# Performance work log

Hardware: AMD Instinct MI355X
Metric: run time of the kernel (lower is better)

## Reference

```python
import jax, jax.numpy as jnp
import numpy as np

N_HEADS = 16


def setup_inputs() -> dict:
    key = jax.random.key(0)
    k1, k2, k3, k4, k5 = jax.random.split(key, 5)
    B, S, D = 2, 2048, 1024
    return {
        "query": jax.random.normal(k1, (B, S, D), dtype=jnp.float32),
        "key": jax.random.normal(k2, (B, S, D), dtype=jnp.float32),
        "value": jax.random.normal(k3, (B, S, D), dtype=jnp.float32),
        "fc_w": jax.random.normal(k4, (D, D), dtype=jnp.float32) * (1.0 / np.sqrt(D)),
        "fc_b": jax.random.normal(k5, (D,), dtype=jnp.float32) * 0.01,
    }


def reference(query, key, value, fc_w, fc_b):
    b, s, d = query.shape
    head_dim = d // N_HEADS
    q = query.reshape(b, s, N_HEADS, head_dim)
    k = key.reshape(b, s, N_HEADS, head_dim)
    v = value.reshape(b, s, N_HEADS, head_dim)
    # energy: [b, n, q, k]
    energy = jnp.einsum('bqnd,bknd->bnqk', q, k)
    scale = 1.0 / jnp.sqrt(jnp.asarray(head_dim, dtype=energy.dtype))
    attn = jax.nn.softmax(energy * scale, axis=3)
    out = jnp.einsum('bnqk,bknd->bqnd', attn, v).reshape(b, s, d)
    # fc: y = x @ W^T + b (torch Linear convention)
    return out @ fc_w.T + fc_b
```

## Files before the change

### kernel.cpp

```cpp
#include <hip/hip_runtime.h>
#include <hip/hip_bf16.h>

#define BATCH 2
#define SEQ 2048
#define DMODEL 1024
#define NHEADS 16
#define HDIM 64
#define KVBLK 64
#define NCHUNK (SEQ / KVBLK)
#define NITER (NCHUNK / 2)

#define QSCALE 0.180336880f
#define DEFER_THR 8.0f

typedef __bf16 bf16x8 __attribute__((ext_vector_type(8)));
typedef __bf16 bf16x4 __attribute__((ext_vector_type(4)));
typedef float f32x4 __attribute__((ext_vector_type(4)));
typedef float f32x16 __attribute__((ext_vector_type(16)));
typedef unsigned int uint2v __attribute__((ext_vector_type(2)));

union B8u { unsigned int u[4]; bf16x8 v; };

__device__ __forceinline__ unsigned int cvt_pk_bf16(float lo, float hi) {
  unsigned int d;
  asm("v_cvt_pk_bf16_f32 %0, %1, %2" : "=v"(d) : "v"(lo), "v"(hi));
  return d;
}

__device__ __forceinline__ void permlane32_swap(unsigned &a, unsigned &b) {
  auto r = __builtin_amdgcn_permlane32_swap(a, b, false, false);
  unsigned tmp[2];
  __builtin_memcpy(tmp, &r, 8);
  a = tmp[0]; b = tmp[1];
}

__global__ __launch_bounds__(256)
void conv_k(const float* __restrict__ K, __bf16* __restrict__ Kbf) {
  const int t = blockIdx.x * 256 + threadIdx.x;
  const int d8 = t & 7, key = (t >> 3) & (SEQ - 1), g = t >> 14;
  const float* src = K + ((size_t)(g >> 4) * SEQ + key) * DMODEL +
                     (g & 15) * HDIM + d8 * 8;
  f32x4 a = *reinterpret_cast<const f32x4*>(src);
  f32x4 c = *reinterpret_cast<const f32x4*>(src + 4);
  bf16x8 o;
#pragma unroll
  for (int j = 0; j < 4; ++j) { o[j] = (__bf16)a[j]; o[4 + j] = (__bf16)c[j]; }
  *reinterpret_cast<bf16x8*>(Kbf + (size_t)t * 8) = o;
}

__global__ __launch_bounds__(256)
void conv_vt(const float* __restrict__ V, __bf16* __restrict__ Vt) {
  const int blk = blockIdx.x;
  const int g = blk >> 5, c0 = (blk & 31) * 64;
  const int b = g >> 4, h = g & 15;
  __shared__ __bf16 T[64][72];

  {
    const int key = threadIdx.x >> 2, dq = threadIdx.x & 3;
    const float* src = V + ((size_t)(b * SEQ) + c0 + key) * DMODEL +
                       h * HDIM + dq * 16;
#pragma unroll
    for (int i = 0; i < 4; ++i) {
      f32x4 v = *reinterpret_cast<const f32x4*>(src + 4 * i);
      bf16x4 o;
#pragma unroll
      for (int j = 0; j < 4; ++j) o[j] = (__bf16)v[j];
      *reinterpret_cast<bf16x4*>(&T[key][dq * 16 + 4 * i]) = o;
    }
  }
  __syncthreads();
  {
    const int d = threadIdx.x >> 2, kq = threadIdx.x & 3;
    bf16x8 r0, r1;
#pragma unroll
    for (int i = 0; i < 8; ++i) {
      r0[i] = T[kq * 16 + i][d];
      r1[i] = T[kq * 16 + 8 + i][d];
    }
    __bf16* dst = Vt + ((size_t)g * HDIM + d) * SEQ + c0 + kq * 16;
    *reinterpret_cast<bf16x8*>(dst) = r0;
    *reinterpret_cast<bf16x8*>(dst + 8) = r1;
  }
}

__global__ __launch_bounds__(256)
void conv_w(const float* __restrict__ W, __bf16* __restrict__ Wbf) {
  const int t = blockIdx.x * 256 + threadIdx.x;
  f32x4 a = *reinterpret_cast<const f32x4*>(W + (size_t)t * 8);
  f32x4 c = *reinterpret_cast<const f32x4*>(W + (size_t)t * 8 + 4);
  bf16x8 o;
#pragma unroll
  for (int j = 0; j < 4; ++j) { o[j] = (__bf16)a[j]; o[4 + j] = (__bf16)c[j]; }
  *reinterpret_cast<bf16x8*>(Wbf + (size_t)t * 8) = o;
}

__global__ __launch_bounds__(512, 4)
void attn_kernel(const float* __restrict__ Q, const __bf16* __restrict__ Kbf,
                 const __bf16* __restrict__ Vt, __bf16* __restrict__ O) {
  const int p = blockIdx.x;
  const int xcd = p & 7, slot = p >> 3;
  const int g = xcd + 8 * (slot >> 4);
  const int b = g >> 4, h = g & 15;
  const int q0 = (slot & 15) * 128;

  const int tid = threadIdx.x;
  const int wave = tid >> 6, lane = tid & 63;
  const int qg = wave & 3, ks = wave >> 2;
  const int l31 = lane & 31, hi = lane >> 5;
  const int ob = hi << 4;
  const int swz = (l31 & 7) << 4;

  __shared__ __align__(16) __bf16 KsA[2][2][64 * 64];
  __shared__ __align__(16) __bf16 VtA[2][2][64 * 64];

  const int qrow = q0 + (qg << 5) + l31;
  const float* qp = Q + ((size_t)(b * SEQ + qrow)) * DMODEL + h * HDIM;
  bf16x8 qf[4];
#pragma unroll
  for (int kd = 0; kd < 4; ++kd) {
    f32x4 a = *reinterpret_cast<const f32x4*>(qp + kd * 16 + hi * 8);
    f32x4 c = *reinterpret_cast<const f32x4*>(qp + kd * 16 + hi * 8 + 4);
#pragma unroll
    for (int j = 0; j < 4; ++j) {
      qf[kd][j]     = (__bf16)(a[j] * QSCALE);
      qf[kd][4 + j] = (__bf16)(c[j] * QSCALE);
    }
  }

  f32x16 oacc0, oacc1;
#pragma unroll
  for (int r = 0; r < 16; ++r) { oacc0[r] = 0.f; oacc1[r] = 0.f; }
  float m_run = -1e30f, l_run = 0.f;

  const __bf16* kgb = Kbf + (size_t)g * SEQ * HDIM;
  const __bf16* vgb = Vt + (size_t)g * HDIM * SEQ;

  const int t2 = tid & 255;
  const int sk_key = t2 >> 2, sk_dq = t2 & 3;
  const int sv_dim = t2 >> 2, sv_kq = t2 & 3;
  const int ksw = (sk_key & 7) << 4;
  const int vsw = (sv_dim & 7) << 4;

  bf16x8 kr0, kr1, vr0, vr1;

#define STAGE_LOAD(C0)                                                        \
  do {                                                                        \
    const __bf16* kc = kgb + (size_t)(C0 + sk_key) * HDIM + sk_dq * 16;       \
    kr0 = *reinterpret_cast<const bf16x8*>(kc);                               \
    kr1 = *reinterpret_cast<const bf16x8*>(kc + 8);                           \
    const __bf16* vc = vgb + (size_t)sv_dim * SEQ + (C0) + sv_kq * 16;        \
    vr0 = *reinterpret_cast<const bf16x8*>(vc);                               \
    vr1 = *reinterpret_cast<const bf16x8*>(vc + 8);                           \
  } while (0)

#define STAGE_WRITE(B)                                                        \
  do {                                                                        \
    char* kdst = (char*)(&KsA[ks][B][0]) + sk_key * 128;                      \
    *reinterpret_cast<bf16x8*>(kdst + (((sk_dq << 5)) ^ ksw)) = kr0;          \
    *reinterpret_cast<bf16x8*>(kdst + (((sk_dq << 5) | 16) ^ ksw)) = kr1;     \
    char* vdst = (char*)(&VtA[ks][B][0]) + sv_dim * 128;                      \
    *reinterpret_cast<bf16x8*>(vdst + (((sv_kq << 5)) ^ vsw)) = vr0;          \
    *reinterpret_cast<bf16x8*>(vdst + (((sv_kq << 5) | 16) ^ vsw)) = vr1;     \
  } while (0)

  STAGE_LOAD(ks * NITER * KVBLK);
  STAGE_WRITE(0);
  __syncthreads();

  for (int i = 0; i < NITER; ++i) {
    const int cur = i & 1;
    const bool pf = (i + 1 < NITER);
    if (pf) STAGE_LOAD((ks * NITER + i + 1) * KVBLK);

    const char* kb = (const char*)(&KsA[ks][cur][0]);
    const char* vb = (const char*)(&VtA[ks][cur][0]);

    f32x16 s0, s1;
#pragma unroll
    for (int r = 0; r < 16; ++r) { s0[r] = 0.f; s1[r] = 0.f; }
    __builtin_amdgcn_s_setprio(1);
#pragma unroll
    for (int kd = 0; kd < 4; ++kd) {
      bf16x8 a0 = *reinterpret_cast<const bf16x8*>(
          kb + l31 * 128 + (((kd << 5) | ob) ^ swz));
      bf16x8 a1 = *reinterpret_cast<const bf16x8*>(
          kb + (32 + l31) * 128 + (((kd << 5) | ob) ^ swz));
      s0 = __builtin_amdgcn_mfma_f32_32x32x16_bf16(a0, qf[kd], s0, 0, 0, 0);
      s1 = __builtin_amdgcn_mfma_f32_32x32x16_bf16(a1, qf[kd], s1, 0, 0, 0);
    }
    __builtin_amdgcn_s_setprio(0);

    float m8[8];
#pragma unroll
    for (int r = 0; r < 8; ++r)
      m8[r] = fmaxf(fmaxf(s0[r], s0[r + 8]), fmaxf(s1[r], s1[r + 8]));
    float pm = fmaxf(fmaxf(fmaxf(m8[0], m8[1]), fmaxf(m8[2], m8[3])),
                     fmaxf(fmaxf(m8[4], m8[5]), fmaxf(m8[6], m8[7])));
    pm = fmaxf(pm, __shfl_xor(pm, 32, 64));

    if (!__all(pm <= m_run + DEFER_THR)) {
      float mu = fmaxf(m_run, pm);
      float al = __builtin_amdgcn_exp2f(m_run - mu);
      m_run = mu;
      l_run *= al;
#pragma unroll
      for (int r = 0; r < 16; ++r) { oacc0[r] *= al; oacc1[r] *= al; }
    }

#pragma unroll
    for (int r = 0; r < 16; ++r) {
      s0[r] = __builtin_amdgcn_exp2f(s0[r] - m_run);
      s1[r] = __builtin_amdgcn_exp2f(s1[r] - m_run);
    }
    float t8[8];
#pragma unroll
    for (int r = 0; r < 8; ++r)
      t8[r] = (s0[r] + s0[r + 8]) + (s1[r] + s1[r + 8]);
    float ts = ((t8[0] + t8[1]) + (t8[2] + t8[3])) +
               ((t8[4] + t8[5]) + (t8[6] + t8[7]));
    ts += __shfl_xor(ts, 32, 64);
    l_run += ts;

    B8u pfr[4];
#pragma unroll
    for (int kq = 0; kq < 4; ++kq) {
      f32x16 ps = (kq < 2) ? s0 : s1;
      const int r0 = (kq & 1) * 8;
      unsigned lo0 = cvt_pk_bf16(ps[r0 + 0], ps[r0 + 1]);
      unsigned lo1 = cvt_pk_bf16(ps[r0 + 2], ps[r0 + 3]);
      unsigned h0  = cvt_pk_bf16(ps[r0 + 4], ps[r0 + 5]);
      unsigned h1  = cvt_pk_bf16(ps[r0 + 6], ps[r0 + 7]);
      permlane32_swap(lo0, h0);
      permlane32_swap(lo1, h1);
      pfr[kq].u[0] = lo0; pfr[kq].u[1] = lo1;
      pfr[kq].u[2] = h0;  pfr[kq].u[3] = h1;
    }

    __builtin_amdgcn_s_setprio(1);
#pragma unroll
    for (int kq = 0; kq < 4; ++kq) {
      bf16x8 v0 = *reinterpret_cast<const bf16x8*>(
          vb + l31 * 128 + (((kq << 5) | ob) ^ swz));
      bf16x8 v1 = *reinterpret_cast<const bf16x8*>(
          vb + (32 + l31) * 128 + (((kq << 5) | ob) ^ swz));
      oacc0 = __builtin_amdgcn_mfma_f32_32x32x16_bf16(v0, pfr[kq].v, oacc0, 0, 0, 0);
      oacc1 = __builtin_amdgcn_mfma_f32_32x32x16_bf16(v1, pfr[kq].v, oacc1, 0, 0, 0);
    }
    __builtin_amdgcn_s_setprio(0);

    if (pf) STAGE_WRITE(cur ^ 1);
    __syncthreads();
  }

  float* Ob = (float*)&KsA[0][0][0];
  float* mb = (float*)&VtA[0][0][0];
  float* lb = mb + 4 * 32;

  if (ks == 1) {
    if (hi == 0) { mb[qg * 32 + l31] = m_run; lb[qg * 32 + l31] = l_run; }
#pragma unroll
    for (int dt = 0; dt < 2; ++dt) {
      f32x16 oa = dt ? oacc1 : oacc0;
#pragma unroll
      for (int r = 0; r < 16; ++r) {
        int dim = dt * 32 + (r & 3) + 8 * (r >> 2) + 4 * hi;
        Ob[(qg * 64 + dim) * 32 + l31] = oa[r];
      }
    }
  }
  __syncthreads();

  if (ks == 0) {
    float m1 = mb[qg * 32 + l31], l1 = lb[qg * 32 + l31];
    float m = fmaxf(m_run, m1);
    float a0 = __builtin_amdgcn_exp2f(m_run - m);
    float a1 = __builtin_amdgcn_exp2f(m1 - m);
    const float inv = 1.0f / (a0 * l_run + a1 * l1);
    __bf16* op = O + ((size_t)(b * SEQ + qrow)) * DMODEL + h * HDIM;
#pragma unroll
    for (int dt = 0; dt < 2; ++dt) {
      f32x16 oa = dt ? oacc1 : oacc0;
#pragma unroll
      for (int a = 0; a < 4; ++a) {
        float e[4];
#pragma unroll
        for (int j = 0; j < 4; ++j) {
          int r = 4 * a + j;
          int dim = dt * 32 + (r & 3) + 8 * (r >> 2) + 4 * hi;
          float opart = Ob[(qg * 64 + dim) * 32 + l31];
          e[j] = (oa[r] * a0 + opart * a1) * inv;
        }
        uint2v w;
        w[0] = cvt_pk_bf16(e[0], e[1]);
        w[1] = cvt_pk_bf16(e[2], e[3]);
        *reinterpret_cast<uint2v*>((char*)op + (dt * 32 + a * 8 + hi * 4) * 2) = w;
      }
    }
  }
#undef STAGE_LOAD
#undef STAGE_WRITE
}

__global__ __launch_bounds__(256)
void fc_kernel(const __bf16* __restrict__ X, const __bf16* __restrict__ W,
               const float* __restrict__ bias, float* __restrict__ Y) {
  const int p = blockIdx.x;
  const int xcd = p & 7, slot = p >> 3;
  const int m0 = (xcd + 8 * (slot >> 3)) * 128;
  const int n0 = (slot & 7) * 128;

  const int tid = threadIdx.x;
  const int wave = tid >> 6, lane = tid & 63;
  const int g = lane >> 4, lr = lane & 15;
  const int wm = wave >> 1, wn = wave & 1;

  __shared__ __bf16 As[128][40];
  __shared__ __bf16 Bs[128][40];

  f32x4 acc[4][4];
#pragma unroll
  for (int i = 0; i < 4; ++i)
#pragma unroll
    for (int j = 0; j < 4; ++j) acc[i][j] = (f32x4){0.f, 0.f, 0.f, 0.f};

  float bv[4];
#pragma unroll
  for (int j = 0; j < 4; ++j) bv[j] = bias[n0 + wn * 64 + 16 * j + lr];

  for (int kk = 0; kk < DMODEL; kk += 32) {
    __syncthreads();
#pragma unroll
    for (int e = 0; e < 2; ++e) {
      int idx = tid + 256 * e;
      int row = idx >> 2, k8 = idx & 3;
      bf16x8 v = *reinterpret_cast<const bf16x8*>(
          X + (size_t)(m0 + row) * DMODEL + kk + k8 * 8);
      *reinterpret_cast<bf16x8*>(&As[row][k8 * 8]) = v;
      bf16x8 w = *reinterpret_cast<const bf16x8*>(
          W + (size_t)(n0 + row) * DMODEL + kk + k8 * 8);
      *reinterpret_cast<bf16x8*>(&Bs[row][k8 * 8]) = w;
    }
    __syncthreads();

    bf16x8 af[4], bfr[4];
#pragma unroll
    for (int i = 0; i < 4; ++i)
      af[i] = *reinterpret_cast<const bf16x8*>(&As[wm * 64 + 16 * i + lr][g * 8]);
#pragma unroll
    for (int j = 0; j < 4; ++j)
      bfr[j] = *reinterpret_cast<const bf16x8*>(&Bs[wn * 64 + 16 * j + lr][g * 8]);
#pragma unroll
    for (int i = 0; i < 4; ++i)
#pragma unroll
      for (int j = 0; j < 4; ++j)
        acc[i][j] = __builtin_amdgcn_mfma_f32_16x16x32_bf16(af[i], bfr[j], acc[i][j], 0, 0, 0);
  }

#pragma unroll
  for (int i = 0; i < 4; ++i) {
    int m = m0 + wm * 64 + 16 * i + g * 4;
#pragma unroll
    for (int j = 0; j < 4; ++j) {
      int n = n0 + wn * 64 + 16 * j + lr;
      float* yp = Y + (size_t)m * DMODEL + n;
#pragma unroll
      for (int r = 0; r < 4; ++r) yp[(size_t)r * DMODEL] = acc[i][j][r] + bv[j];
    }
  }
}

extern "C" void kernel_launch(void* const* d_in, const int* in_sizes, int n_in,
                              void* d_out, int out_size, void* d_ws, size_t ws_size,
                              hipStream_t stream) {
  const float* q    = (const float*)d_in[0];
  const float* k    = (const float*)d_in[1];
  const float* v    = (const float*)d_in[2];
  const float* w    = (const float*)d_in[3];
  const float* bias = (const float*)d_in[4];
  float* out = (float*)d_out;

  char* ws = (char*)d_ws;
  __bf16* O   = (__bf16*)(ws);
  __bf16* Kbf = (__bf16*)(ws + (8u << 20));
  __bf16* Vt  = (__bf16*)(ws + (16u << 20));
  __bf16* Wbf = (__bf16*)(ws + (24u << 20));

  conv_k<<<dim3(2048), 256, 0, stream>>>(k, Kbf);
  conv_vt<<<dim3(1024), 256, 0, stream>>>(v, Vt);
  conv_w<<<dim3(512), 256, 0, stream>>>(w, Wbf);
  attn_kernel<<<dim3(512), 512, 0, stream>>>(q, Kbf, Vt, O);
  fc_kernel<<<dim3(256), 256, 0, stream>>>(O, Wbf, bias, out);
}
```

Measured before the change: 95.13 us.

## Merge conversion kernels into one launch and retile fc GEMM to 128x64

Folds the three fp32-to-bf16 conversion kernels (K, transposed V, W) into one kernel that dispatches on block index, removing two launches and their inter-kernel gaps. The fc GEMM tile drops from 128x128 to 128x64 with a K step of 64 instead of 32, doubling the grid to 512 blocks so more CUs are busy and halving the number of barrier-separated iterations. In exchange, each fc block reuses less data per tile, and the merged conversion kernel reserves shared memory even for blocks that do not need it.

After: 85.14 us (median of 2 runs). 1.12x faster.

```diff
diff --git a/kernel.cpp b/kernel.cpp
--- a/kernel.cpp
+++ b/kernel.cpp
@@ -35,63 +35,62 @@
 }
 
 __global__ __launch_bounds__(256)
-void conv_k(const float* __restrict__ K, __bf16* __restrict__ Kbf) {
-  const int t = blockIdx.x * 256 + threadIdx.x;
-  const int d8 = t & 7, key = (t >> 3) & (SEQ - 1), g = t >> 14;
-  const float* src = K + ((size_t)(g >> 4) * SEQ + key) * DMODEL +
-                     (g & 15) * HDIM + d8 * 8;
-  f32x4 a = *reinterpret_cast<const f32x4*>(src);
-  f32x4 c = *reinterpret_cast<const f32x4*>(src + 4);
-  bf16x8 o;
-#pragma unroll
-  for (int j = 0; j < 4; ++j) { o[j] = (__bf16)a[j]; o[4 + j] = (__bf16)c[j]; }
-  *reinterpret_cast<bf16x8*>(Kbf + (size_t)t * 8) = o;
-}
-
-__global__ __launch_bounds__(256)
-void conv_vt(const float* __restrict__ V, __bf16* __restrict__ Vt) {
-  const int blk = blockIdx.x;
-  const int g = blk >> 5, c0 = (blk & 31) * 64;
-  const int b = g >> 4, h = g & 15;
+void conv_all(const float* __restrict__ K, __bf16* __restrict__ Kbf,
+              const float* __restrict__ V, __bf16* __restrict__ Vt,
+              const float* __restrict__ W, __bf16* __restrict__ Wbf) {
+  const int p = blockIdx.x;
   __shared__ __bf16 T[64][72];
 
-  {
-    const int key = threadIdx.x >> 2, dq = threadIdx.x & 3;
-    const float* src = V + ((size_t)(b * SEQ) + c0 + key) * DMODEL +
-                       h * HDIM + dq * 16;
-#pragma unroll
-    for (int i = 0; i < 4; ++i) {
-      f32x4 v = *reinterpret_cast<const f32x4*>(src + 4 * i);
-      bf16x4 o;
-#pragma unroll
-      for (int j = 0; j < 4; ++j) o[j] = (__bf16)v[j];
-      *reinterpret_cast<bf16x4*>(&T[key][dq * 16 + 4 * i]) = o;
-    }
-  }
-  __syncthreads();
-  {
-    const int d = threadIdx.x >> 2, kq = threadIdx.x & 3;
-    bf16x8 r0, r1;
-#pragma unroll
-    for (int i = 0; i < 8; ++i) {
-      r0[i] = T[kq * 16 + i][d];
-      r1[i] = T[kq * 16 + 8 + i][d];
-    }
-    __bf16* dst = Vt + ((size_t)g * HDIM + d) * SEQ + c0 + kq * 16;
-    *reinterpret_cast<bf16x8*>(dst) = r0;
-    *reinterpret_cast<bf16x8*>(dst + 8) = r1;
-  }
-}
-
-__global__ __launch_bounds__(256)
-void conv_w(const float* __restrict__ W, __bf16* __restrict__ Wbf) {
-  const int t = blockIdx.x * 256 + threadIdx.x;
-  f32x4 a = *reinterpret_cast<const f32x4*>(W + (size_t)t * 8);
-  f32x4 c = *reinterpret_cast<const f32x4*>(W + (size_t)t * 8 + 4);
-  bf16x8 o;
-#pragma unroll
-  for (int j = 0; j < 4; ++j) { o[j] = (__bf16)a[j]; o[4 + j] = (__bf16)c[j]; }
-  *reinterpret_cast<bf16x8*>(Wbf + (size_t)t * 8) = o;
+  if (p < 2048) {
+    const int t = p * 256 + threadIdx.x;
+    const int d8 = t & 7, key = (t >> 3) & (SEQ - 1), g = t >> 14;
+    const float* src = K + ((size_t)(g >> 4) * SEQ + key) * DMODEL +
+                       (g & 15) * HDIM + d8 * 8;
+    f32x4 a = *reinterpret_cast<const f32x4*>(src);
+    f32x4 c = *reinterpret_cast<const f32x4*>(src + 4);
+    bf16x8 o;
+#pragma unroll
+    for (int j = 0; j < 4; ++j) { o[j] = (__bf16)a[j]; o[4 + j] = (__bf16)c[j]; }
+    *reinterpret_cast<bf16x8*>(Kbf + (size_t)t * 8) = o;
+  } else if (p < 3072) {
+    const int blk = p - 2048;
+    const int g = blk >> 5, c0 = (blk & 31) * 64;
+    const int b = g >> 4, h = g & 15;
+    {
+      const int key = threadIdx.x >> 2, dq = threadIdx.x & 3;
+      const float* src = V + ((size_t)(b * SEQ) + c0 + key) * DMODEL +
+                         h * HDIM + dq * 16;
+#pragma unroll
+      for (int i = 0; i < 4; ++i) {
+        f32x4 v = *reinterpret_cast<const f32x4*>(src + 4 * i);
+        bf16x4 o;
+#pragma unroll
+        for (int j = 0; j < 4; ++j) o[j] = (__bf16)v[j];
+        *reinterpret_cast<bf16x4*>(&T[key][dq * 16 + 4 * i]) = o;
+      }
+    }
+    __syncthreads();
+    {
+      const int d = threadIdx.x >> 2, kq = threadIdx.x & 3;
+      bf16x8 r0, r1;
+#pragma unroll
+      for (int i = 0; i < 8; ++i) {
+        r0[i] = T[kq * 16 + i][d];
+        r1[i] = T[kq * 16 + 8 + i][d];
+      }
+      __bf16* dst = Vt + ((size_t)g * HDIM + d) * SEQ + c0 + kq * 16;
+      *reinterpret_cast<bf16x8*>(dst) = r0;
+      *reinterpret_cast<bf16x8*>(dst + 8) = r1;
+    }
+  } else {
+    const int t = (p - 3072) * 256 + threadIdx.x;
+    f32x4 a = *reinterpret_cast<const f32x4*>(W + (size_t)t * 8);
+    f32x4 c = *reinterpret_cast<const f32x4*>(W + (size_t)t * 8 + 4);
+    bf16x8 o;
+#pragma unroll
+    for (int j = 0; j < 4; ++j) { o[j] = (__bf16)a[j]; o[4 + j] = (__bf16)c[j]; }
+    *reinterpret_cast<bf16x8*>(Wbf + (size_t)t * 8) = o;
+  }
 }
 
 __global__ __launch_bounds__(512, 4)
@@ -306,62 +305,73 @@
                const float* __restrict__ bias, float* __restrict__ Y) {
   const int p = blockIdx.x;
   const int xcd = p & 7, slot = p >> 3;
-  const int m0 = (xcd + 8 * (slot >> 3)) * 128;
-  const int n0 = (slot & 7) * 128;
+  const int m0 = (xcd + 8 * (slot >> 4)) * 128;
+  const int n0 = (slot & 15) * 64;
 
   const int tid = threadIdx.x;
   const int wave = tid >> 6, lane = tid & 63;
   const int g = lane >> 4, lr = lane & 15;
   const int wm = wave >> 1, wn = wave & 1;
 
-  __shared__ __bf16 As[128][40];
-  __shared__ __bf16 Bs[128][40];
-
-  f32x4 acc[4][4];
+  __shared__ __bf16 As[128][72];
+  __shared__ __bf16 Bs[64][72];
+
+  f32x4 acc[4][2];
 #pragma unroll
   for (int i = 0; i < 4; ++i)
 #pragma unroll
-    for (int j = 0; j < 4; ++j) acc[i][j] = (f32x4){0.f, 0.f, 0.f, 0.f};
-
-  float bv[4];
-#pragma unroll
-  for (int j = 0; j < 4; ++j) bv[j] = bias[n0 + wn * 64 + 16 * j + lr];
-
-  for (int kk = 0; kk < DMODEL; kk += 32) {
+    for (int j = 0; j < 2; ++j) acc[i][j] = (f32x4){0.f, 0.f, 0.f, 0.f};
+
+  float bv[2];
+#pragma unroll
+  for (int j = 0; j < 2; ++j) bv[j] = bias[n0 + wn * 32 + 16 * j + lr];
+
+  for (int kk = 0; kk < DMODEL; kk += 64) {
     __syncthreads();
 #pragma unroll
-    for (int e = 0; e < 2; ++e) {
+    for (int e = 0; e < 4; ++e) {
       int idx = tid + 256 * e;
-      int row = idx >> 2, k8 = idx & 3;
+      int row = idx >> 3, k8 = idx & 7;
       bf16x8 v = *reinterpret_cast<const bf16x8*>(
           X + (size_t)(m0 + row) * DMODEL + kk + k8 * 8);
       *reinterpret_cast<bf16x8*>(&As[row][k8 * 8]) = v;
+    }
+#pragma unroll
+    for (int e = 0; e < 2; ++e) {
+      int idx = tid + 256 * e;
+      int row = idx >> 3, k8 = idx & 7;
       bf16x8 w = *reinterpret_cast<const bf16x8*>(
           W + (size_t)(n0 + row) * DMODEL + kk + k8 * 8);
       *reinterpret_cast<bf16x8*>(&Bs[row][k8 * 8]) = w;
     }
     __syncthreads();
 
-    bf16x8 af[4], bfr[4];
-#pragma unroll
-    for (int i = 0; i < 4; ++i)
-      af[i] = *reinterpret_cast<const bf16x8*>(&As[wm * 64 + 16 * i + lr][g * 8]);
-#pragma unroll
-    for (int j = 0; j < 4; ++j)
-      bfr[j] = *reinterpret_cast<const bf16x8*>(&Bs[wn * 64 + 16 * j + lr][g * 8]);
-#pragma unroll
-    for (int i = 0; i < 4; ++i)
-#pragma unroll
-      for (int j = 0; j < 4; ++j)
-        acc[i][j] = __builtin_amdgcn_mfma_f32_16x16x32_bf16(af[i], bfr[j], acc[i][j], 0, 0, 0);
+#pragma unroll
+    for (int ks2 = 0; ks2 < 2; ++ks2) {
+      bf16x8 af[4], bfr[2];
+#pragma unroll
+      for (int i = 0; i < 4; ++i)
+        af[i] = *reinterpret_cast<const bf16x8*>(
+            &As[wm * 64 + 16 * i + lr][ks2 * 32 + g * 8]);
+#pragma unroll
+      for (int j = 0; j < 2; ++j)
+        bfr[j] = *reinterpret_cast<const bf16x8*>(
+            &Bs[wn * 32 + 16 * j + lr][ks2 * 32 + g * 8]);
+#pragma unroll
+      for (int i = 0; i < 4; ++i)
+#pragma unroll
+        for (int j = 0; j < 2; ++j)
+          acc[i][j] = __builtin_amdgcn_mfma_f32_16x16x32_bf16(
+              af[i], bfr[j], acc[i][j], 0, 0, 0);
+    }
   }
 
 #pragma unroll
   for (int i = 0; i < 4; ++i) {
     int m = m0 + wm * 64 + 16 * i + g * 4;
 #pragma unroll
-    for (int j = 0; j < 4; ++j) {
-      int n = n0 + wn * 64 + 16 * j + lr;
+    for (int j = 0; j < 2; ++j) {
+      int n = n0 + wn * 32 + 16 * j + lr;
       float* yp = Y + (size_t)m * DMODEL + n;
 #pragma unroll
       for (int r = 0; r < 4; ++r) yp[(size_t)r * DMODEL] = acc[i][j][r] + bv[j];
@@ -385,9 +395,7 @@
   __bf16* Vt  = (__bf16*)(ws + (16u << 20));
   __bf16* Wbf = (__bf16*)(ws + (24u << 20));
 
-  conv_k<<<dim3(2048), 256, 0, stream>>>(k, Kbf);
-  conv_vt<<<dim3(1024), 256, 0, stream>>>(v, Vt);
-  conv_w<<<dim3(512), 256, 0, stream>>>(w, Wbf);
+  conv_all<<<dim3(3584), 256, 0, stream>>>(k, Kbf, v, Vt, w, Wbf);
   attn_kernel<<<dim3(512), 512, 0, stream>>>(q, Kbf, Vt, O);
-  fc_kernel<<<dim3(256), 256, 0, stream>>>(O, Wbf, bias, out);
-}
+  fc_kernel<<<dim3(512), 256, 0, stream>>>(O, Wbf, bias, out);
+}
```
